# Kernel tuning notes

Hardware: AMD Instinct MI355X
Metric: run time of the kernel (lower is better)

## Reference

```python
import jax, jax.numpy as jnp
import numpy as np

N_NODES = 100000
N_EDGES = 1600000
IN_C = 128
HID = 128
LAT = 64
N_LAYERS = 3
N_GRAPHS = 1000


def setup_inputs() -> dict:
    key = jax.random.key(0)
    ks = jax.random.split(key, 16)
    x = jax.random.normal(ks[0], (N_NODES, IN_C), dtype=jnp.float32)
    edge_index = jax.random.randint(ks[1], (2, N_EDGES), 0, N_NODES, dtype=jnp.int64)
    batch = jnp.sort(jax.random.randint(ks[2], (N_NODES,), 0, N_GRAPHS, dtype=jnp.int64))
    s = 1.0 / np.sqrt(HID)
    # per-layer GIN MLP params (in_c == hidden for all layers since IN_C == HID)
    W1 = jax.random.normal(ks[3], (N_LAYERS, IN_C, HID), dtype=jnp.float32) * s
    b1 = jnp.zeros((N_LAYERS, HID), dtype=jnp.float32)
    W2 = jax.random.normal(ks[4], (N_LAYERS, HID, HID), dtype=jnp.float32) * s
    b2 = jnp.zeros((N_LAYERS, HID), dtype=jnp.float32)
    W_mu = jax.random.normal(ks[5], (HID, LAT), dtype=jnp.float32) * s
    b_mu = jnp.zeros((LAT,), dtype=jnp.float32)
    W_lv = jax.random.normal(ks[6], (HID, LAT), dtype=jnp.float32) * s
    b_lv = jnp.zeros((LAT,), dtype=jnp.float32)
    return {"x": x, "edge_index": edge_index, "batch": batch,
            "W1": W1, "b1": b1, "W2": W2, "b2": b2,
            "W_mu": W_mu, "b_mu": b_mu, "W_lv": W_lv, "b_lv": b_lv}


def reference(x, edge_index, batch, W1, b1, W2, b2, W_mu, b_mu, W_lv, b_lv):
    src, dst = edge_index[0], edge_index[1]
    h = x
    for i in range(N_LAYERS):
        # GINConv (eps=0): h' = MLP(h + sum_{j in N(i)} h_j); scatter-add over edges
        agg = h + jax.ops.segment_sum(h[src], dst, num_segments=N_NODES)
        h = jax.nn.relu(agg @ W1[i] + b1[i])
        h = jax.nn.relu(h @ W2[i] + b2[i])
        h = jax.nn.relu(h)  # extra ReLU in forward after conv (idempotent here)
    # global_add_pool: segment-sum nodes into graphs
    g = jax.ops.segment_sum(h, batch, num_segments=N_GRAPHS)  # [G, HID]
    mu = g @ W_mu + b_mu
    logvar = g @ W_lv + b_lv
    return (mu, logvar)
```

## Files before the change

kernel.cpp:

```cpp
#include <hip/hip_runtime.h>

#define N_NODES 100000
#define N_EDGES 1600000
#define HID 128
#define LAT 64
#define N_LAYERS 3
#define N_GRAPHS 1000
#define CAP 64
#define NBIN 391
#define MAXBIN 4608
#define ACHUNK 8192
#define ABLOCKS ((N_EDGES + ACHUNK - 1) / ACHUNK)
#define CVT_BLOCKS (N_NODES * HID / 4 / 256)

typedef short bf16x8 __attribute__((ext_vector_type(8)));
typedef float f32x4 __attribute__((ext_vector_type(4)));

__device__ __forceinline__ float bf2f(unsigned short h) {
    union { unsigned int u; float f; } c;
    c.u = ((unsigned int)h) << 16;
    return c.f;
}
__device__ __forceinline__ unsigned short f2bf(float f) {
    union { float f; unsigned int u; } c;
    c.f = f;
    unsigned int u = c.u;
    return (unsigned short)((u + 0x7fffu + ((u >> 16) & 1u)) >> 16);
}
__device__ __forceinline__ unsigned int pack2(float a, float b) {
    return (unsigned int)f2bf(a) | ((unsigned int)f2bf(b) << 16);
}
__device__ __forceinline__ void addrow(float* acc, uint4 w) {
    acc[0] += bf2f((unsigned short)w.x); acc[1] += bf2f((unsigned short)(w.x >> 16));
    acc[2] += bf2f((unsigned short)w.y); acc[3] += bf2f((unsigned short)(w.y >> 16));
    acc[4] += bf2f((unsigned short)w.z); acc[5] += bf2f((unsigned short)(w.z >> 16));
    acc[6] += bf2f((unsigned short)w.w); acc[7] += bf2f((unsigned short)(w.w >> 16));
}

__global__ __launch_bounds__(256) void setup_kernel(const int* __restrict__ ei,
                                                    int* __restrict__ gcnt,
                                                    unsigned int* __restrict__ ebin,
                                                    const float* __restrict__ x,
                                                    unsigned short* __restrict__ xb,
                                                    const float* __restrict__ W1,
                                                    const float* __restrict__ W2,
                                                    unsigned short* __restrict__ Wt) {
    __shared__ unsigned int scount[NBIN];
    __shared__ unsigned int sfill[NBIN];
    int t = threadIdx.x;
    int blk = blockIdx.x;
    if (blk >= ABLOCKS) {
        int b2 = blk - ABLOCKS;
        if (b2 < 6) {
            const float* W = ((b2 & 1) ? W2 : W1) + (size_t)(b2 >> 1) * HID * HID;
            unsigned short* D = Wt + (size_t)b2 * HID * HID;
            for (int idx = t; idx < HID * HID; idx += 256) {
                int n = idx >> 7, k = idx & 127;
                D[n * HID + k] = f2bf(W[k * HID + n]);
            }
            return;
        }
        int i = (b2 - 6) * 256 + t;
        if (i >= N_NODES * HID / 4) return;
        float4 v = ((const float4*)x)[i];
        ((uint2*)xb)[i] = make_uint2(pack2(v.x, v.y), pack2(v.z, v.w));
        return;
    }
    int base = blk * ACHUNK;
    int n = N_EDGES - base;
    if (n > ACHUNK) n = ACHUNK;
    for (int i = t; i < NBIN; i += 256) scount[i] = 0u;
    __syncthreads();
    for (int i = t; i < n; i += 256) {
        int d = ei[N_EDGES + base + i];
        atomicAdd(&scount[d >> 8], 1u);
    }
    __syncthreads();
    for (int b = t; b < NBIN; b += 256) {
        unsigned int c = scount[b];
        sfill[b] = c ? (unsigned int)atomicAdd(&gcnt[b], (int)c) : 0u;
    }
    __syncthreads();
    for (int i = t; i < n; i += 256) {
        int s = ei[base + i];
        int d = ei[N_EDGES + base + i];
        int b = d >> 8;
        unsigned int pos = atomicAdd(&sfill[b], 1u);
        ebin[(size_t)b * MAXBIN + pos] = ((unsigned int)(d & 255) << 24) | (unsigned int)s;
    }
}

__global__ __launch_bounds__(256) void binB_kernel(const unsigned int* __restrict__ ebin,
                                                   const int* __restrict__ gcnt,
                                                   int* __restrict__ cnt,
                                                   int* __restrict__ csr) {
    __shared__ int lcsr[128][CAP];
    __shared__ int scnt[128];
    int blk = blockIdx.x;
    int b = blk >> 1;
    int half = blk & 1;
    int t = threadIdx.x;
    if (t < 128) scnt[t] = 0;
    __syncthreads();
    int c = gcnt[b];
    const unsigned int* src = ebin + (size_t)b * MAXBIN;
    for (int i = t; i < c; i += 256) {
        unsigned int e = src[i];
        int dl = (int)(e >> 24);
        if ((dl >> 7) == half) {
            int slot = atomicAdd(&scnt[dl & 127], 1);
            lcsr[dl & 127][slot] = (int)(e & 0xFFFFFFu);
        }
    }
    __syncthreads();
    int n0 = (b << 8) + (half << 7);
    if (t < 128 && n0 + t < N_NODES) cnt[n0 + t] = scnt[t];
    int nv = N_NODES - n0;
    if (nv > 128) nv = 128;
    if (nv < 0) nv = 0;
    int4* dst = (int4*)(csr + (size_t)n0 * CAP);
    const int4* ls = (const int4*)&lcsr[0][0];
    for (int i = t; i < nv * (CAP / 4); i += 256) dst[i] = ls[i];
}

__global__ __launch_bounds__(256) void gather_kernel(const unsigned short* __restrict__ h,
                                                     const int* __restrict__ cnt,
                                                     const int* __restrict__ csr,
                                                     unsigned short* __restrict__ agg) {
    int t = threadIdx.x;
    int node = blockIdx.x * 16 + (t >> 4);
    int q = t & 15;
    if (node >= N_NODES) return;
    const int* nl = csr + (size_t)node * CAP;
    int deg = cnt[node];
    float acc[8] = {0.f, 0.f, 0.f, 0.f, 0.f, 0.f, 0.f, 0.f};
    addrow(acc, *(const uint4*)(h + (size_t)node * HID + q * 8));
    int e = 0;
    for (; e + 8 <= deg; e += 8) {
        int s0 = nl[e], s1 = nl[e + 1], s2 = nl[e + 2], s3 = nl[e + 3];
        int s4 = nl[e + 4], s5 = nl[e + 5], s6 = nl[e + 6], s7 = nl[e + 7];
        uint4 w0 = *(const uint4*)(h + (size_t)s0 * HID + q * 8);
        uint4 w1 = *(const uint4*)(h + (size_t)s1 * HID + q * 8);
        uint4 w2 = *(const uint4*)(h + (size_t)s2 * HID + q * 8);
        uint4 w3 = *(const uint4*)(h + (size_t)s3 * HID + q * 8);
        uint4 w4 = *(const uint4*)(h + (size_t)s4 * HID + q * 8);
        uint4 w5 = *(const uint4*)(h + (size_t)s5 * HID + q * 8);
        uint4 w6 = *(const uint4*)(h + (size_t)s6 * HID + q * 8);
        uint4 w7 = *(const uint4*)(h + (size_t)s7 * HID + q * 8);
        addrow(acc, w0); addrow(acc, w1); addrow(acc, w2); addrow(acc, w3);
        addrow(acc, w4); addrow(acc, w5); addrow(acc, w6); addrow(acc, w7);
    }
    for (; e + 4 <= deg; e += 4) {
        int s0 = nl[e], s1 = nl[e + 1], s2 = nl[e + 2], s3 = nl[e + 3];
        uint4 w0 = *(const uint4*)(h + (size_t)s0 * HID + q * 8);
        uint4 w1 = *(const uint4*)(h + (size_t)s1 * HID + q * 8);
        uint4 w2 = *(const uint4*)(h + (size_t)s2 * HID + q * 8);
        uint4 w3 = *(const uint4*)(h + (size_t)s3 * HID + q * 8);
        addrow(acc, w0); addrow(acc, w1); addrow(acc, w2); addrow(acc, w3);
    }
    for (; e < deg; ++e) {
        addrow(acc, *(const uint4*)(h + (size_t)nl[e] * HID + q * 8));
    }
    uint4 o;
    o.x = pack2(acc[0], acc[1]);
    o.y = pack2(acc[2], acc[3]);
    o.z = pack2(acc[4], acc[5]);
    o.w = pack2(acc[6], acc[7]);
    *(uint4*)(agg + (size_t)node * HID + q * 8) = o;
}

__global__ __launch_bounds__(256) void mlp_kernel(const unsigned short* __restrict__ A,
                                                  const unsigned short* __restrict__ W1t,
                                                  const float* __restrict__ b1,
                                                  const unsigned short* __restrict__ W2t,
                                                  const float* __restrict__ b2,
                                                  unsigned short* __restrict__ out,
                                                  const int* __restrict__ batch,
                                                  float* __restrict__ gpool) {
    __shared__ unsigned short sA[64][136];
    __shared__ unsigned short sW[128][40];
    __shared__ float sb[128];
    __shared__ int sbatch[64];
    const int t = threadIdx.x;
    const int w = t >> 6;
    const int l = t & 63;
    const int lm = l & 15;
    const int quad = l >> 4;
    const int row0 = blockIdx.x * 64;

    for (int idx = t; idx < 1024; idx += 256) {
        int r = idx >> 4, c = idx & 15;
        int grow = row0 + r;
        uint4 v = make_uint4(0u, 0u, 0u, 0u);
        if (grow < N_NODES) v = *(const uint4*)(A + (size_t)grow * HID + c * 8);
        *(uint4*)&sA[r][c * 8] = v;
    }
    if (gpool && t < 64) {
        int n = row0 + t;
        sbatch[t] = (n < N_NODES) ? batch[n] : -1;
    }

    const unsigned short* Wt2[2] = {W1t, W2t};
    const float* bias[2] = {b1, b2};

    const int n_0 = t >> 2;
    const int n_1 = (t >> 2) + 64;
    const int kq = t & 3;
    uint4 rw0 = *(const uint4*)(W1t + (size_t)n_0 * HID + kq * 8);
    uint4 rw1 = *(const uint4*)(W1t + (size_t)n_1 * HID + kq * 8);

    for (int p = 0; p < 2; ++p) {
        if (t < 128) sb[t] = bias[p][t];
        f32x4 acc[8];
#pragma unroll
        for (int nt = 0; nt < 8; ++nt) acc[nt] = (f32x4){0.f, 0.f, 0.f, 0.f};

        for (int kc = 0; kc < 4; ++kc) {
            __syncthreads();
            *(uint4*)&sW[n_0][kq * 8] = rw0;
            *(uint4*)&sW[n_1][kq * 8] = rw1;
            __syncthreads();
            int s = (p << 2) + kc;
            if (s < 7) {
                int pn = (s + 1) >> 2, kn = (s + 1) & 3;
                const unsigned short* Wn = Wt2[pn];
                rw0 = *(const uint4*)(Wn + (size_t)n_0 * HID + kn * 32 + kq * 8);
                rw1 = *(const uint4*)(Wn + (size_t)n_1 * HID + kn * 32 + kq * 8);
            }
            bf16x8 a = *(const bf16x8*)&sA[w * 16 + lm][kc * 32 + quad * 8];
#pragma unroll
            for (int nt = 0; nt < 8; ++nt) {
                bf16x8 b = *(const bf16x8*)&sW[nt * 16 + lm][quad * 8];
                acc[nt] = __builtin_amdgcn_mfma_f32_16x16x32_bf16(a, b, acc[nt], 0, 0, 0);
            }
        }
        __syncthreads();
#pragma unroll
        for (int nt = 0; nt < 8; ++nt) {
            float bv = sb[nt * 16 + lm];
#pragma unroll
            for (int r = 0; r < 4; ++r) {
                int m = w * 16 + quad * 4 + r;
                float val = fmaxf(acc[nt][r] + bv, 0.f);
                sA[m][nt * 16 + lm] = f2bf(val);
            }
        }
        __syncthreads();
    }

    if (!gpool) {
        for (int idx = t; idx < 1024; idx += 256) {
            int r = idx >> 4, c = idx & 15;
            int grow = row0 + r;
            if (grow < N_NODES)
                *(uint4*)(out + (size_t)grow * HID + c * 8) = *(const uint4*)&sA[r][c * 8];
        }
    } else {
        int c = t & 127;
        int r0 = (t >> 7) * 32;
        float acc = 0.f;
        int cur = sbatch[r0];
        for (int r = r0; r < r0 + 32; ++r) {
            int b = sbatch[r];
            if (b < 0) break;
            if (b != cur) {
                atomicAdd(&gpool[(size_t)cur * HID + c], acc);
                acc = 0.f;
                cur = b;
            }
            acc += bf2f(sA[r][c]);
        }
        if (cur >= 0) atomicAdd(&gpool[(size_t)cur * HID + c], acc);
    }
}

__global__ __launch_bounds__(128) void head_kernel(const float* __restrict__ g,
                                                   const float* __restrict__ Wmu,
                                                   const float* __restrict__ bmu,
                                                   const float* __restrict__ Wlv,
                                                   const float* __restrict__ blv,
                                                   float* __restrict__ out) {
    __shared__ float sg[HID];
    int gi = blockIdx.x;
    sg[threadIdx.x] = g[(size_t)gi * HID + threadIdx.x];
    __syncthreads();
    int j = threadIdx.x & 63;
    bool is_lv = threadIdx.x >= 64;
    const float* W = is_lv ? Wlv : Wmu;
    float acc = is_lv ? blv[j] : bmu[j];
    for (int k = 0; k < HID; ++k) acc = fmaf(sg[k], W[k * LAT + j], acc);
    out[(is_lv ? (size_t)N_GRAPHS * LAT : 0) + (size_t)gi * LAT + j] = acc;
}

extern "C" void kernel_launch(void* const* d_in, const int* in_sizes, int n_in,
                              void* d_out, int out_size, void* d_ws, size_t ws_size,
                              hipStream_t stream) {
    const float* x     = (const float*)d_in[0];
    const int*   ei    = (const int*)d_in[1];
    const int*   batch = (const int*)d_in[2];
    const float* W1    = (const float*)d_in[3];
    const float* b1    = (const float*)d_in[4];
    const float* W2    = (const float*)d_in[5];
    const float* b2    = (const float*)d_in[6];
    const float* Wmu   = (const float*)d_in[7];
    const float* bmu   = (const float*)d_in[8];
    const float* Wlv   = (const float*)d_in[9];
    const float* blv   = (const float*)d_in[10];
    float* out = (float*)d_out;

    unsigned short* xb   = (unsigned short*)d_ws;
    unsigned short* agg  = xb + (size_t)N_NODES * HID;
    unsigned short* hbuf = agg + (size_t)N_NODES * HID;
    int* csr = (int*)(hbuf + (size_t)N_NODES * HID);
    unsigned int* ebin = (unsigned int*)(csr + (size_t)N_NODES * CAP);
    unsigned short* Wt = (unsigned short*)(ebin + (size_t)NBIN * MAXBIN);
    float* g  = (float*)(Wt + (size_t)6 * HID * HID);
    int* gcnt = (int*)(g + (size_t)N_GRAPHS * HID);
    int* cnt  = gcnt + NBIN + 1;

    hipMemsetAsync(g, 0, (size_t)N_GRAPHS * HID * sizeof(float) + (NBIN + 1) * sizeof(int),
                   stream);

    setup_kernel<<<ABLOCKS + 6 + CVT_BLOCKS, 256, 0, stream>>>(ei, gcnt, ebin,
                                                               x, xb, W1, W2, Wt);
    binB_kernel<<<NBIN * 2, 256, 0, stream>>>(ebin, gcnt, cnt, csr);

    const unsigned short* hcur = xb;
    for (int i = 0; i < N_LAYERS; ++i) {
        bool last = (i == N_LAYERS - 1);
        gather_kernel<<<(N_NODES + 15) / 16, 256, 0, stream>>>(hcur, cnt, csr, agg);
        mlp_kernel<<<(N_NODES + 63) / 64, 256, 0, stream>>>(
            agg, Wt + (size_t)(2 * i) * HID * HID, b1 + (size_t)i * HID,
            Wt + (size_t)(2 * i + 1) * HID * HID, b2 + (size_t)i * HID, hbuf,
            batch, last ? g : nullptr);
        hcur = hbuf;
    }
    head_kernel<<<N_GRAPHS, 128, 0, stream>>>(g, Wmu, bmu, Wlv, blv, out);
}
```

Measured before the change: 408.6 us.

## Keep MLP weights in registers and split output columns across waves

```diff
diff --git a/kernel.cpp b/kernel.cpp
--- a/kernel.cpp
+++ b/kernel.cpp
@@ -178,8 +178,6 @@
                                                   const int* __restrict__ batch,
                                                   float* __restrict__ gpool) {
     __shared__ unsigned short sA[64][136];
-    __shared__ unsigned short sW[128][40];
-    __shared__ float sb[128];
     __shared__ int sbatch[64];
     const int t = threadIdx.x;
     const int w = t >> 6;
@@ -187,66 +185,96 @@
     const int lm = l & 15;
     const int quad = l >> 4;
     const int row0 = blockIdx.x * 64;
-
-    for (int idx = t; idx < 1024; idx += 256) {
-        int r = idx >> 4, c = idx & 15;
-        int grow = row0 + r;
-        uint4 v = make_uint4(0u, 0u, 0u, 0u);
-        if (grow < N_NODES) v = *(const uint4*)(A + (size_t)grow * HID + c * 8);
-        *(uint4*)&sA[r][c * 8] = v;
-    }
+    const int n0 = w * 32 + lm;
+    const int n1 = w * 32 + 16 + lm;
+
+    bf16x8 B0[4], B1f[4];
+#pragma unroll
+    for (int kc = 0; kc < 4; ++kc) {
+        B0[kc]  = *(const bf16x8*)(W1t + (size_t)n0 * HID + kc * 32 + quad * 8);
+        B1f[kc] = *(const bf16x8*)(W1t + (size_t)n1 * HID + kc * 32 + quad * 8);
+    }
+    float bv10 = b1[n0], bv11 = b1[n1];
+    float bv20 = b2[n0], bv21 = b2[n1];
+
     if (gpool && t < 64) {
         int n = row0 + t;
         sbatch[t] = (n < N_NODES) ? batch[n] : -1;
     }
 
-    const unsigned short* Wt2[2] = {W1t, W2t};
-    const float* bias[2] = {b1, b2};
-
-    const int n_0 = t >> 2;
-    const int n_1 = (t >> 2) + 64;
-    const int kq = t & 3;
-    uint4 rw0 = *(const uint4*)(W1t + (size_t)n_0 * HID + kq * 8);
-    uint4 rw1 = *(const uint4*)(W1t + (size_t)n_1 * HID + kq * 8);
-
-    for (int p = 0; p < 2; ++p) {
-        if (t < 128) sb[t] = bias[p][t];
-        f32x4 acc[8];
-#pragma unroll
-        for (int nt = 0; nt < 8; ++nt) acc[nt] = (f32x4){0.f, 0.f, 0.f, 0.f};
-
+    f32x4 acc[4][2];
+#pragma unroll
+    for (int rt = 0; rt < 4; ++rt) {
+        acc[rt][0] = (f32x4){0.f, 0.f, 0.f, 0.f};
+        acc[rt][1] = (f32x4){0.f, 0.f, 0.f, 0.f};
+    }
+#pragma unroll
+    for (int rt = 0; rt < 4; ++rt) {
+        int grow = row0 + rt * 16 + lm;
+        bf16x8 a[4];
+        if (grow < N_NODES) {
+            const unsigned short* ap = A + (size_t)grow * HID + quad * 8;
+#pragma unroll
+            for (int kc = 0; kc < 4; ++kc) a[kc] = *(const bf16x8*)(ap + kc * 32);
+        } else {
+#pragma unroll
+            for (int kc = 0; kc < 4; ++kc) a[kc] = (bf16x8){0, 0, 0, 0, 0, 0, 0, 0};
+        }
+#pragma unroll
         for (int kc = 0; kc < 4; ++kc) {
-            __syncthreads();
-            *(uint4*)&sW[n_0][kq * 8] = rw0;
-            *(uint4*)&sW[n_1][kq * 8] = rw1;
-            __syncthreads();
-            int s = (p << 2) + kc;
-            if (s < 7) {
-                int pn = (s + 1) >> 2, kn = (s + 1) & 3;
-                const unsigned short* Wn = Wt2[pn];
-                rw0 = *(const uint4*)(Wn + (size_t)n_0 * HID + kn * 32 + kq * 8);
-                rw1 = *(const uint4*)(Wn + (size_t)n_1 * HID + kn * 32 + kq * 8);
-            }
-            bf16x8 a = *(const bf16x8*)&sA[w * 16 + lm][kc * 32 + quad * 8];
-#pragma unroll
-            for (int nt = 0; nt < 8; ++nt) {
-                bf16x8 b = *(const bf16x8*)&sW[nt * 16 + lm][quad * 8];
-                acc[nt] = __builtin_amdgcn_mfma_f32_16x16x32_bf16(a, b, acc[nt], 0, 0, 0);
-            }
-        }
-        __syncthreads();
-#pragma unroll
-        for (int nt = 0; nt < 8; ++nt) {
-            float bv = sb[nt * 16 + lm];
-#pragma unroll
-            for (int r = 0; r < 4; ++r) {
-                int m = w * 16 + quad * 4 + r;
-                float val = fmaxf(acc[nt][r] + bv, 0.f);
-                sA[m][nt * 16 + lm] = f2bf(val);
-            }
-        }
-        __syncthreads();
-    }
+            acc[rt][0] = __builtin_amdgcn_mfma_f32_16x16x32_bf16(a[kc], B0[kc], acc[rt][0], 0, 0, 0);
+            acc[rt][1] = __builtin_amdgcn_mfma_f32_16x16x32_bf16(a[kc], B1f[kc], acc[rt][1], 0, 0, 0);
+        }
+    }
+
+#pragma unroll
+    for (int rt = 0; rt < 4; ++rt) {
+#pragma unroll
+        for (int r = 0; r < 4; ++r) {
+            int m = rt * 16 + quad * 4 + r;
+            sA[m][n0] = f2bf(fmaxf(acc[rt][0][r] + bv10, 0.f));
+            sA[m][n1] = f2bf(fmaxf(acc[rt][1][r] + bv11, 0.f));
+        }
+    }
+    __syncthreads();
+
+    bf16x8 C0[4], C1v[4];
+#pragma unroll
+    for (int kc = 0; kc < 4; ++kc) {
+        C0[kc]  = *(const bf16x8*)(W2t + (size_t)n0 * HID + kc * 32 + quad * 8);
+        C1v[kc] = *(const bf16x8*)(W2t + (size_t)n1 * HID + kc * 32 + quad * 8);
+    }
+
+    f32x4 acc2[4][2];
+#pragma unroll
+    for (int rt = 0; rt < 4; ++rt) {
+        acc2[rt][0] = (f32x4){0.f, 0.f, 0.f, 0.f};
+        acc2[rt][1] = (f32x4){0.f, 0.f, 0.f, 0.f};
+    }
+#pragma unroll
+    for (int rt = 0; rt < 4; ++rt) {
+        bf16x8 a[4];
+#pragma unroll
+        for (int kc = 0; kc < 4; ++kc)
+            a[kc] = *(const bf16x8*)&sA[rt * 16 + lm][kc * 32 + quad * 8];
+#pragma unroll
+        for (int kc = 0; kc < 4; ++kc) {
+            acc2[rt][0] = __builtin_amdgcn_mfma_f32_16x16x32_bf16(a[kc], C0[kc], acc2[rt][0], 0, 0, 0);
+            acc2[rt][1] = __builtin_amdgcn_mfma_f32_16x16x32_bf16(a[kc], C1v[kc], acc2[rt][1], 0, 0, 0);
+        }
+    }
+    __syncthreads();
+
+#pragma unroll
+    for (int rt = 0; rt < 4; ++rt) {
+#pragma unroll
+        for (int r = 0; r < 4; ++r) {
+            int m = rt * 16 + quad * 4 + r;
+            sA[m][n0] = f2bf(fmaxf(acc2[rt][0][r] + bv20, 0.f));
+            sA[m][n1] = f2bf(fmaxf(acc2[rt][1][r] + bv21, 0.f));
+        }
+    }
+    __syncthreads();
 
     if (!gpool) {
         for (int idx = t; idx < 1024; idx += 256) {
@@ -258,19 +286,19 @@
     } else {
         int c = t & 127;
         int r0 = (t >> 7) * 32;
-        float acc = 0.f;
+        float acc3 = 0.f;
         int cur = sbatch[r0];
         for (int r = r0; r < r0 + 32; ++r) {
             int b = sbatch[r];
             if (b < 0) break;
             if (b != cur) {
-                atomicAdd(&gpool[(size_t)cur * HID + c], acc);
-                acc = 0.f;
+                atomicAdd(&gpool[(size_t)cur * HID + c], acc3);
+                acc3 = 0.f;
                 cur = b;
             }
-            acc += bf2f(sA[r][c]);
-        }
-        if (cur >= 0) atomicAdd(&gpool[(size_t)cur * HID + c], acc);
+            acc3 += bf2f(sA[r][c]);
+        }
+        if (cur >= 0) atomicAdd(&gpool[(size_t)cur * HID + c], acc3);
     }
 }
 
```

Result: slower. 430.8 us (+5.5%).
